# Kernel tuning notes

Hardware: AMD Instinct MI355X
Metric: run time of the kernel (lower is better)

## Reference

```python
import jax, jax.numpy as jnp
import numpy as np

KS = 7      # kernel_size
PAD = 3     # padding
G = 8       # groups
CIN = 64    # inplanes
COUT = 64   # outplanes
DD = COUT // G        # channels per group = 8
REL = DD // 2         # rel_size = 4


def group_conv1x1(x, w, b):
    # x: (b, C, H, W), w: (G, out_per_g, in_per_g)
    bsz, c, h, ww = x.shape
    xg = x.reshape(bsz, G, c // G, h, ww)
    y = jnp.einsum('bgihw,goi->bgohw', xg, w).reshape(bsz, -1, h, ww)
    if b is not None:
        y = y + b[None, :, None, None]
    return y


def unfold_windows(xp, h, w):
    # xp: (b, C, h+2*PAD, w+2*PAD) -> (b, C, h, w, KS*KS), window flattened (kh, kw)
    return jnp.stack([xp[:, :, i:i + h, j:j + w]
                      for i in range(KS) for j in range(KS)], axis=-1)


def setup_inputs() -> dict:
    key = jax.random.key(0)
    ks = jax.random.split(key, 8)
    x = jax.random.normal(ks[0], (4, CIN, 56, 56), dtype=jnp.float32)
    wq = jax.random.normal(ks[1], (G, DD, CIN // G), dtype=jnp.float32) * 0.1
    wk = jax.random.normal(ks[2], (G, DD, CIN // G), dtype=jnp.float32) * 0.1
    bk = jax.random.normal(ks[3], (COUT,), dtype=jnp.float32) * 0.1
    wv = jax.random.normal(ks[4], (G, DD, CIN // G), dtype=jnp.float32) * 0.1
    bv = jax.random.normal(ks[5], (COUT,), dtype=jnp.float32) * 0.1
    rel_x = jax.random.normal(ks[6], (REL, KS, 1), dtype=jnp.float32)
    rel_y = jax.random.normal(ks[7], (REL, 1, KS), dtype=jnp.float32)
    return {"x": x, "wq": wq, "wk": wk, "bk": bk, "wv": wv, "bv": bv,
            "rel_x": rel_x, "rel_y": rel_y}


def reference(x, wq, wk, bk, wv, bv, rel_x, rel_y):
    b, d, h, w = x.shape
    q = group_conv1x1(x, wq, None)                      # (b, COUT, h, w)
    x_pad = jnp.pad(x, ((0, 0), (0, 0), (PAD, PAD), (PAD, PAD)))
    k = group_conv1x1(x_pad, wk, bk)
    v = group_conv1x1(x_pad, wv, bv)
    kw = unfold_windows(k, h, w).reshape(b, G, DD, h, w, KS * KS)
    vw = unfold_windows(v, h, w).reshape(b, G, DD, h, w, KS * KS)
    qg = q.reshape(b, G, DD, h, w)
    q_x, q_y = qg[:, :, :REL], qg[:, :, REL:]
    rx = jnp.broadcast_to(rel_x, (REL, KS, KS)).reshape(REL, -1)  # (REL, 49)
    ry = jnp.broadcast_to(rel_y, (REL, KS, KS)).reshape(REL, -1)
    qr = jnp.concatenate([jnp.einsum('bgdhw,dk->bgdhwk', q_x, rx),
                          jnp.einsum('bgdhw,dk->bgdhwk', q_y, ry)], axis=2)
    logits = qg[..., None] * kw + qr                    # (b, G, DD, h, w, 49)
    soft = jax.nn.softmax(logits, axis=-1)
    out = jnp.sum(soft * vw, axis=-1).reshape(b, -1, h, w)
    return out
```

## Files before the change

kernel.cpp:

```cpp
#include <hip/hip_runtime.h>
#include <math.h>

#define KS    7
#define PADW  3
#define H     56
#define W     56
#define HW    (H * W)
#define TILE  8
#define PATCH 14
#define PPOS  (PATCH * PATCH)

#if __has_builtin(__builtin_amdgcn_exp2f)
#define EXP2F(x) __builtin_amdgcn_exp2f(x)
#else
#define EXP2F(x) exp2f(x)
#endif
#if __has_builtin(__builtin_amdgcn_rcpf)
#define RCPF(x) __builtin_amdgcn_rcpf(x)
#else
#define RCPF(x) (1.0f / (x))
#endif

#define LOG2E 1.44269504088896340736f

__global__ __launch_bounds__(256, 8) void attn_fused(
    const float* __restrict__ x,
    const float* __restrict__ wq,
    const float* __restrict__ wk,
    const float* __restrict__ bk,
    const float* __restrict__ wv,
    const float* __restrict__ bv,
    const float* __restrict__ rel_x,
    const float* __restrict__ rel_y,
    float* __restrict__ out)
{
    __shared__ float2 kvm[8][PPOS];

    const int tid  = threadIdx.x;
    const int tile = blockIdx.x;
    const int bz   = blockIdx.y;
    const int b    = bz >> 3;
    const int g    = bz & 7;
    const int c0   = g * 8;

    const int tileY = tile / 7;
    const int tileX = tile - tileY * 7;
    const int h0 = tileY * TILE;
    const int w0 = tileX * TILE;

    const float* wqg = wq + g * 64;
    const float* wkg = wk + g * 64;
    const float* wvg = wv + g * 64;
    const float* xg  = x + (size_t)(b * 64 + c0) * HW;

    if (tid < PPOS) {
        const int py = tid / PATCH;
        const int px = tid - py * PATCH;
        const int oy = h0 + py - PADW;
        const int ox = w0 + px - PADW;
        const bool in = (oy >= 0) & (oy < H) & (ox >= 0) & (ox < W);
        const float* xp = xg + oy * W + ox;
        float xv[8];
#pragma unroll
        for (int i = 0; i < 8; ++i)
            xv[i] = in ? xp[i * HW] : 0.f;
#pragma unroll
        for (int dch = 0; dch < 8; ++dch) {
            float ka = bk[c0 + dch];
            float va = bv[c0 + dch];
#pragma unroll
            for (int i = 0; i < 8; ++i) {
                ka = fmaf(xv[i], wkg[dch * 8 + i], ka);
                va = fmaf(xv[i], wvg[dch * 8 + i], va);
            }
            kvm[dch][tid] = make_float2(ka, va);
        }
    }
    __syncthreads();

    const int pix  = tid & 63;
    const int dsel = tid >> 6;
    const int ty   = pix >> 3;
    const int tx   = pix & 7;
    const int h    = h0 + ty;
    const int w    = w0 + tx;

    const float* xcp = xg + h * W + w;
    float xc[8];
#pragma unroll
    for (int i = 0; i < 8; ++i)
        xc[i] = xcp[i * HW];

    const int base = ty * PATCH + tx;

#pragma unroll
    for (int half = 0; half < 2; ++half) {
        const int dch = half * 4 + dsel;

        float qv = 0.f;
#pragma unroll
        for (int i = 0; i < 8; ++i)
            qv = fmaf(xc[i], wqg[dch * 8 + i], qv);
        const float qv2 = qv * LOG2E;

        float qvr2[7];
#pragma unroll
        for (int i = 0; i < 7; ++i) {
            float r = (half == 0) ? rel_x[dch * 7 + i]
                                  : rel_y[(dch - 4) * 7 + i];
            qvr2[i] = qv2 * r;
        }

        const float2* kp = &kvm[dch][base];

        float l = 0.f, acc = 0.f;
#pragma unroll
        for (int i = 0; i < 7; ++i) {
            float li = 0.f, ai = 0.f;
#pragma unroll
            for (int j = 0; j < 7; ++j) {
                float2 kv = kp[i * PATCH + j];
                float addv = (half == 0) ? qvr2[i] : qvr2[j];
                float e = EXP2F(fmaf(qv2, kv.x, addv));
                li += e;
                ai = fmaf(e, kv.y, ai);
            }
            l += li;
            acc += ai;
        }

        out[((size_t)(b * 64 + c0 + dch) * H + h) * W + w] = acc * RCPF(l);
    }
}

extern "C" void kernel_launch(void* const* d_in, const int* in_sizes, int n_in,
                              void* d_out, int out_size, void* d_ws, size_t ws_size,
                              hipStream_t stream) {
    const float* x     = (const float*)d_in[0];
    const float* wq    = (const float*)d_in[1];
    const float* wk    = (const float*)d_in[2];
    const float* bk    = (const float*)d_in[3];
    const float* wv    = (const float*)d_in[4];
    const float* bv    = (const float*)d_in[5];
    const float* rel_x = (const float*)d_in[6];
    const float* rel_y = (const float*)d_in[7];

    dim3 grid(49, 32, 1);
    attn_fused<<<grid, dim3(256), 0, stream>>>(
        x, wq, wk, bk, wv, bv, rel_x, rel_y, (float*)d_out);
}
```

Baseline: 83.05 us.

## Split QKV projection into a precompute kernel writing padded K/V and Q to workspace

```diff
diff --git a/kernel.cpp b/kernel.cpp
--- a/kernel.cpp
+++ b/kernel.cpp
@@ -1,14 +1,21 @@
 #include <hip/hip_runtime.h>
 #include <math.h>
 
-#define KS    7
-#define PADW  3
-#define H     56
-#define W     56
-#define HW    (H * W)
-#define TILE  8
-#define PATCH 14
-#define PPOS  (PATCH * PATCH)
+#define KS     7
+#define PADW   3
+#define H      56
+#define W      56
+#define HW     (H * W)
+#define TILE   8
+#define PATCH  14
+#define PPOS   (PATCH * PATCH)
+#define PADH   62
+#define KVROW  64
+#define KVPLN  (PADH * KVROW)
+#define KVGRP  (8 * KVPLN)
+#define NPADPIX (PADH * PADH)
+#define QOFF_FLOATS (32 * KVGRP * 2)
+#define QGRP  (8 * HW)
 
 #if __has_builtin(__builtin_amdgcn_exp2f)
 #define EXP2F(x) __builtin_amdgcn_exp2f(x)
@@ -23,13 +30,69 @@
 
 #define LOG2E 1.44269504088896340736f
 
-__global__ __launch_bounds__(256, 8) void attn_fused(
+__global__ __launch_bounds__(256) void qkv_pre(
     const float* __restrict__ x,
     const float* __restrict__ wq,
     const float* __restrict__ wk,
     const float* __restrict__ bk,
     const float* __restrict__ wv,
     const float* __restrict__ bv,
+    float2* __restrict__ kvg,
+    float* __restrict__ qg)
+{
+    const int tid = threadIdx.x;
+    const int bg  = blockIdx.y;
+    const int b   = bg >> 3;
+    const int g   = bg & 7;
+    const int c0  = g * 8;
+
+    const int p = blockIdx.x * 256 + tid;
+    if (p >= NPADPIX) return;
+    const int py = p / PADH;
+    const int px = p - py * PADH;
+    const int oy = py - PADW;
+    const int ox = px - PADW;
+    const bool in = (oy >= 0) & (oy < H) & (ox >= 0) & (ox < W);
+
+    const float* xg  = x + (size_t)(b * 64 + c0) * HW + oy * W + ox;
+    float xv[8];
+#pragma unroll
+    for (int i = 0; i < 8; ++i)
+        xv[i] = in ? xg[i * HW] : 0.f;
+
+    const float* wqg = wq + g * 64;
+    const float* wkg = wk + g * 64;
+    const float* wvg = wv + g * 64;
+
+    float2* kvb = kvg + (size_t)bg * KVGRP + py * KVROW + px;
+#pragma unroll
+    for (int dch = 0; dch < 8; ++dch) {
+        float ka = bk[c0 + dch];
+        float va = bv[c0 + dch];
+#pragma unroll
+        for (int i = 0; i < 8; ++i) {
+            ka = fmaf(xv[i], wkg[dch * 8 + i], ka);
+            va = fmaf(xv[i], wvg[dch * 8 + i], va);
+        }
+        kvb[dch * KVPLN] = make_float2(ka, va);
+    }
+
+    if (in) {
+        float* qb = qg + (size_t)bg * QGRP + oy * W + ox;
+#pragma unroll
+        for (int dch = 0; dch < 8; ++dch) {
+            float qa = 0.f;
+#pragma unroll
+            for (int i = 0; i < 8; ++i)
+                qa = fmaf(xv[i], wqg[dch * 8 + i], qa);
+            qb[dch * HW] = qa;
+        }
+    }
+}
+
+__global__ __launch_bounds__(256) void attn_fused(
+    const float2* __restrict__ kvg,
+    const float* __restrict__ qg,
     const float* __restrict__ rel_x,
     const float* __restrict__ rel_y,
     float* __restrict__ out)
@@ -38,9 +101,9 @@
 
     const int tid  = threadIdx.x;
     const int tile = blockIdx.x;
-    const int bz   = blockIdx.y;
-    const int b    = bz >> 3;
-    const int g    = bz & 7;
+    const int bg   = blockIdx.y;
+    const int b    = bg >> 3;
+    const int g    = bg & 7;
     const int c0   = g * 8;
 
     const int tileY = tile / 7;
@@ -48,33 +111,13 @@
     const int h0 = tileY * TILE;
     const int w0 = tileX * TILE;
 
-    const float* wqg = wq + g * 64;
-    const float* wkg = wk + g * 64;
-    const float* wvg = wv + g * 64;
-    const float* xg  = x + (size_t)(b * 64 + c0) * HW;
-
-    if (tid < PPOS) {
-        const int py = tid / PATCH;
-        const int px = tid - py * PATCH;
-        const int oy = h0 + py - PADW;
-        const int ox = w0 + px - PADW;
-        const bool in = (oy >= 0) & (oy < H) & (ox >= 0) & (ox < W);
-        const float* xp = xg + oy * W + ox;
-        float xv[8];
-#pragma unroll
-        for (int i = 0; i < 8; ++i)
-            xv[i] = in ? xp[i * HW] : 0.f;
-#pragma unroll
-        for (int dch = 0; dch < 8; ++dch) {
-            float ka = bk[c0 + dch];
-            float va = bv[c0 + dch];
-#pragma unroll
-            for (int i = 0; i < 8; ++i) {
-                ka = fmaf(xv[i], wkg[dch * 8 + i], ka);
-                va = fmaf(xv[i], wvg[dch * 8 + i], va);
-            }
-            kvm[dch][tid] = make_float2(ka, va);
-        }
+    const float2* kvb = kvg + (size_t)bg * KVGRP;
+    for (int idx = tid; idx < 8 * PPOS; idx += 256) {
+        const int dch = idx / PPOS;
+        const int pp  = idx - dch * PPOS;
+        const int py  = pp / PATCH;
+        const int px  = pp - py * PATCH;
+        (&kvm[0][0])[idx] = kvb[dch * KVPLN + (h0 + py) * KVROW + (w0 + px)];
     }
     __syncthreads();
 
@@ -84,23 +127,15 @@
     const int tx   = pix & 7;
     const int h    = h0 + ty;
     const int w    = w0 + tx;
+    const int base = ty * PATCH + tx;
 
-    const float* xcp = xg + h * W + w;
-    float xc[8];
-#pragma unroll
-    for (int i = 0; i < 8; ++i)
-        xc[i] = xcp[i * HW];
-
-    const int base = ty * PATCH + tx;
+    const float* qb = qg + (size_t)bg * QGRP + h * W + w;
 
 #pragma unroll
     for (int half = 0; half < 2; ++half) {
         const int dch = half * 4 + dsel;
 
-        float qv = 0.f;
-#pragma unroll
-        for (int i = 0; i < 8; ++i)
-            qv = fmaf(xc[i], wqg[dch * 8 + i], qv);
+        const float qv  = qb[dch * HW];
         const float qv2 = qv * LOG2E;
 
         float qvr2[7];
@@ -145,7 +180,12 @@
     const float* rel_x = (const float*)d_in[6];
     const float* rel_y = (const float*)d_in[7];
 
-    dim3 grid(49, 32, 1);
-    attn_fused<<<grid, dim3(256), 0, stream>>>(
-        x, wq, wk, bk, wv, bv, rel_x, rel_y, (float*)d_out);
+    float2* kvg = (float2*)d_ws;
+    float*  qg  = (float*)d_ws + QOFF_FLOATS;
+
+    dim3 g1((NPADPIX + 255) / 256, 32, 1);
+    qkv_pre<<<g1, dim3(256), 0, stream>>>(x, wq, wk, bk, wv, bv, kvg, qg);
+
+    dim3 g2(49, 32, 1);
+    attn_fused<<<g2, dim3(256), 0, stream>>>(kvg, qg, rel_x, rel_y, (float*)d_out);
 }
```

Result: slower. 91.67 us (+10.4%).

## Enlarge tiles to 14x8 and compute two vertical pixels per thread sharing K/V loads

Applied to the files above, without the earlier changes.

```diff
diff --git a/kernel.cpp b/kernel.cpp
--- a/kernel.cpp
+++ b/kernel.cpp
@@ -6,9 +6,11 @@
 #define H     56
 #define W     56
 #define HW    (H * W)
-#define TILE  8
-#define PATCH 14
-#define PPOS  (PATCH * PATCH)
+#define TW    8
+#define TH    14
+#define PW    14
+#define PH    20
+#define PPOS  (PH * PW)
 
 #if __has_builtin(__builtin_amdgcn_exp2f)
 #define EXP2F(x) __builtin_amdgcn_exp2f(x)
@@ -23,7 +25,7 @@
 
 #define LOG2E 1.44269504088896340736f
 
-__global__ __launch_bounds__(256, 8) void attn_fused(
+__global__ __launch_bounds__(256, 4) void attn_fused(
     const float* __restrict__ x,
     const float* __restrict__ wq,
     const float* __restrict__ wk,
@@ -38,24 +40,24 @@
 
     const int tid  = threadIdx.x;
     const int tile = blockIdx.x;
-    const int bz   = blockIdx.y;
-    const int b    = bz >> 3;
-    const int g    = bz & 7;
+    const int bg   = blockIdx.y;
+    const int b    = bg >> 3;
+    const int g    = bg & 7;
     const int c0   = g * 8;
 
     const int tileY = tile / 7;
     const int tileX = tile - tileY * 7;
-    const int h0 = tileY * TILE;
-    const int w0 = tileX * TILE;
+    const int h0 = tileY * TH;
+    const int w0 = tileX * TW;
 
     const float* wqg = wq + g * 64;
     const float* wkg = wk + g * 64;
     const float* wvg = wv + g * 64;
     const float* xg  = x + (size_t)(b * 64 + c0) * HW;
 
-    if (tid < PPOS) {
-        const int py = tid / PATCH;
-        const int px = tid - py * PATCH;
+    for (int idx = tid; idx < PPOS; idx += 256) {
+        const int py = idx / PW;
+        const int px = idx - py * PW;
         const int oy = h0 + py - PADW;
         const int ox = w0 + px - PADW;
         const bool in = (oy >= 0) & (oy < H) & (ox >= 0) & (ox < W);
@@ -73,63 +75,86 @@
                 ka = fmaf(xv[i], wkg[dch * 8 + i], ka);
                 va = fmaf(xv[i], wvg[dch * 8 + i], va);
             }
-            kvm[dch][tid] = make_float2(ka, va);
+            kvm[dch][idx] = make_float2(ka, va);
         }
     }
     __syncthreads();
 
-    const int pix  = tid & 63;
     const int dsel = tid >> 6;
-    const int ty   = pix >> 3;
-    const int tx   = pix & 7;
-    const int h    = h0 + ty;
-    const int w    = w0 + tx;
+    const int p    = tid & 63;
+    const int rp   = p >> 3;
+    const int tx   = p & 7;
 
-    const float* xcp = xg + h * W + w;
-    float xc[8];
+    if (rp < 7) {
+        const int y0 = 2 * rp;
+        const int ha = h0 + y0;
+        const int w  = w0 + tx;
+
+        const float* xcp = xg + ha * W + w;
+        float xc0[8], xc1[8];
 #pragma unroll
-    for (int i = 0; i < 8; ++i)
-        xc[i] = xcp[i * HW];
+        for (int i = 0; i < 8; ++i) {
+            xc0[i] = xcp[i * HW];
+            xc1[i] = xcp[i * HW + W];
+        }
 
-    const int base = ty * PATCH + tx;
+        const float2* kbase0 = &kvm[0][y0 * PW + tx];
 
 #pragma unroll
-    for (int half = 0; half < 2; ++half) {
-        const int dch = half * 4 + dsel;
+        for (int half = 0; half < 2; ++half) {
+            const int dch = half * 4 + dsel;
 
-        float qv = 0.f;
+            float qv0 = 0.f, qv1 = 0.f;
 #pragma unroll
-        for (int i = 0; i < 8; ++i)
-            qv = fmaf(xc[i], wqg[dch * 8 + i], qv);
-        const float qv2 = qv * LOG2E;
+            for (int i = 0; i < 8; ++i) {
+                qv0 = fmaf(xc0[i], wqg[dch * 8 + i], qv0);
+                qv1 = fmaf(xc1[i], wqg[dch * 8 + i], qv1);
+            }
+            const float q20 = qv0 * LOG2E;
+            const float q21 = qv1 * LOG2E;
 
-        float qvr2[7];
+            float r0[7], r1[7];
 #pragma unroll
-        for (int i = 0; i < 7; ++i) {
-            float r = (half == 0) ? rel_x[dch * 7 + i]
-                                  : rel_y[(dch - 4) * 7 + i];
-            qvr2[i] = qv2 * r;
+            for (int i = 0; i < 7; ++i) {
+                const float r = (half == 0) ? rel_x[dch * 7 + i]
+                                            : rel_y[(dch - 4) * 7 + i];
+                r0[i] = q20 * r;
+                r1[i] = q21 * r;
+            }
+
+            const float2* kp = kbase0 + dch * PPOS;
+
+            float l0 = 0.f, a0 = 0.f, l1 = 0.f, a1 = 0.f;
+#pragma unroll
+            for (int r = 0; r < 8; ++r) {
+                float2 kv[7];
+#pragma unroll
+                for (int j = 0; j < 7; ++j)
+                    kv[j] = kp[r * PW + j];
+                if (r < 7) {
+#pragma unroll
+                    for (int j = 0; j < 7; ++j) {
+                        const float addv = (half == 0) ? r0[r] : r0[j];
+                        const float e = EXP2F(fmaf(q20, kv[j].x, addv));
+                        l0 += e;
+                        a0 = fmaf(e, kv[j].y, a0);
+                    }
+                }
+                if (r >= 1) {
+#pragma unroll
+                    for (int j = 0; j < 7; ++j) {
+                        const float addv = (half == 0) ? r1[r - 1] : r1[j];
+                        const float e = EXP2F(fmaf(q21, kv[j].x, addv));
+                        l1 += e;
+                        a1 = fmaf(e, kv[j].y, a1);
+                    }
+                }
+            }
+
+            float* op = out + ((size_t)(b * 64 + c0 + dch) * H + ha) * W + w;
+            op[0] = a0 * RCPF(l0);
+            op[W] = a1 * RCPF(l1);
         }
-
-        const float2* kp = &kvm[dch][base];
-
-        float l = 0.f, acc = 0.f;
-#pragma unroll
-        for (int i = 0; i < 7; ++i) {
-            float li = 0.f, ai = 0.f;
-#pragma unroll
-            for (int j = 0; j < 7; ++j) {
-                float2 kv = kp[i * PATCH + j];
-                float addv = (half == 0) ? qvr2[i] : qvr2[j];
-                float e = EXP2F(fmaf(qv2, kv.x, addv));
-                li += e;
-                ai = fmaf(e, kv.y, ai);
-            }
-            l += li;
-            acc += ai;
-        }
-
-        out[((size_t)(b * 64 + c0 + dch) * H + h) * W + w] = acc * RCPF(l);
     }
 }
 
@@ -145,7 +170,7 @@
     const float* rel_x = (const float*)d_in[6];
     const float* rel_y = (const float*)d_in[7];
 
-    dim3 grid(49, 32, 1);
+    dim3 grid(28, 32, 1);
     attn_fused<<<grid, dim3(256), 0, stream>>>(
         x, wq, wk, bk, wv, bv, rel_x, rel_y, (float*)d_out);
 }
```

After: 82.63 us. About the same (-0.5%).
